# Kernel tuning notes

Measured on AMD Instinct MI355X. Metric: run time of the kernel, lower is better.

The kernel has to match this reference:

```python
import jax, jax.numpy as jnp
import numpy as np

N_NODES = 100000


def gcn_conv(x, edge_index, W, b):
    """PyG GCNConv: add self-loops, symmetric deg^-1/2 normalization, linear."""
    n = x.shape[0]
    h = x @ W  # [N, out]
    loop = jnp.arange(n, dtype=edge_index.dtype)
    src = jnp.concatenate([edge_index[0], loop])
    dst = jnp.concatenate([edge_index[1], loop])
    deg = jax.ops.segment_sum(jnp.ones_like(dst, dtype=h.dtype), dst, num_segments=n)
    dinv = jnp.where(deg > 0, jax.lax.rsqrt(deg), 0.0)
    norm = dinv[src] * dinv[dst]  # [E+N]
    msg = h[src] * norm[:, None]  # gather + scale
    out = jax.ops.segment_sum(msg, dst, num_segments=n)  # scatter-add
    return out + b


def setup_inputs() -> dict:
    key = jax.random.key(0)
    k1, k2, k3, k4 = jax.random.split(key, 4)
    d_in, d_hid, d_out = 128, 128, 128  # output_dim // 2 = 128
    E = 1600000
    x = jax.random.normal(k1, (N_NODES, d_in), dtype=jnp.float32)
    edge_index = jax.random.randint(k2, (2, E), 0, N_NODES, dtype=jnp.int64)
    s1 = 1.0 / np.sqrt(d_in)
    s2 = 1.0 / np.sqrt(d_hid)
    W1 = jax.random.normal(k3, (d_in, d_hid), dtype=jnp.float32) * s1
    b1 = jnp.zeros((d_hid,), dtype=jnp.float32)
    W2 = jax.random.normal(k4, (d_hid, d_out), dtype=jnp.float32) * s2
    b2 = jnp.zeros((d_out,), dtype=jnp.float32)
    return {"x": x, "edge_index": edge_index, "W1": W1, "b1": b1, "W2": W2, "b2": b2}


def reference(x, edge_index, W1, b1, W2, b2):
    h = jax.nn.relu(gcn_conv(x, edge_index, W1, b1))
    # dropout(p=0.5) is identity in eval mode
    return gcn_conv(h, edge_index, W2, b2)
```

## Files before the change

### kernel.cpp

```cpp
#include <hip/hip_runtime.h>

#define D 128

typedef unsigned int uint;
typedef unsigned short ushort;
typedef __attribute__((ext_vector_type(8))) short bf16x8_t;
typedef __attribute__((ext_vector_type(4))) float f32x4_t;

#define NB 128
#define BSH 7
#define BMASK 127
#define MAXBUCK 1024

__global__ __launch_bounds__(256) void kp_hist(const int* __restrict__ dst,
                                               int* __restrict__ table,
                                               int E, int nbuck, int chunk) {
    __shared__ int h[MAXBUCK];
    int t = threadIdx.x, b = blockIdx.x;
    for (int i = t; i < nbuck; i += 256) h[i] = 0;
    __syncthreads();
    int s = b * chunk, e = min(E, s + chunk);
    for (int i = s + t; i < e; i += 256)
        atomicAdd(&h[dst[i] >> BSH], 1);
    __syncthreads();
    for (int i = t; i < nbuck; i += 256)
        table[i * NB + b] = h[i];
}

__global__ void kp_scan_table(int* __restrict__ table, int* __restrict__ btot) {
    __shared__ int s[NB];
    int t = threadIdx.x, b = blockIdx.x;
    int v = table[b * NB + t];
    s[t] = v; __syncthreads();
    for (int off = 1; off < NB; off <<= 1) {
        int x = (t >= off) ? s[t - off] : 0;
        __syncthreads();
        s[t] += x;
        __syncthreads();
    }
    table[b * NB + t] = s[t] - v;
    if (t == NB - 1) btot[b] = s[t];
}

__global__ void kp_scan_btot(const int* __restrict__ btot, int* __restrict__ bucketBase,
                             int* __restrict__ row_ptr, int nbuck, int E, int n) {
    __shared__ int s[1024];
    int t = threadIdx.x;
    int v = (t < nbuck) ? btot[t] : 0;
    s[t] = v; __syncthreads();
    for (int off = 1; off < 1024; off <<= 1) {
        int x = (t >= off) ? s[t - off] : 0;
        __syncthreads();
        s[t] += x;
        __syncthreads();
    }
    if (t < nbuck) bucketBase[t] = s[t] - v;
    if (t == 0) { bucketBase[nbuck] = E; row_ptr[n] = E; }
}

__global__ __launch_bounds__(256) void kp_scatter(const int* __restrict__ src,
                                                  const int* __restrict__ dst,
                                                  const int* __restrict__ table,
                                                  const int* __restrict__ bucketBase,
                                                  uint* __restrict__ sorted,
                                                  int E, int nbuck, int chunk) {
    __shared__ int off[MAXBUCK];
    int t = threadIdx.x, b = blockIdx.x;
    for (int i = t; i < nbuck; i += 256)
        off[i] = bucketBase[i] + table[i * NB + b];
    __syncthreads();
    int s = b * chunk, e = min(E, s + chunk);
    for (int i = s + t; i < e; i += 256) {
        int d = dst[i];
        int bk = d >> BSH;
        int slot = atomicAdd(&off[bk], 1);
        sorted[slot] = ((uint)src[i] << BSH) | (uint)(d & BMASK);
    }
}

__global__ __launch_bounds__(256) void kp_build(const uint* __restrict__ sorted,
                                                const int* __restrict__ bucketBase,
                                                int* __restrict__ row_ptr,
                                                int* __restrict__ col,
                                                float* __restrict__ dinv, int n) {
    __shared__ int cnt[128], loc[128], cnt2[128];
    int t = threadIdx.x, b = blockIdx.x;
    int base = bucketBase[b], end = bucketBase[b + 1];
    if (t < 128) { cnt[t] = 0; cnt2[t] = 0; }
    __syncthreads();
    for (int i = base + t; i < end; i += 256)
        atomicAdd(&cnt[sorted[i] & BMASK], 1);
    __syncthreads();
    int v = (t < 128) ? cnt[t] : 0;
    if (t < 128) loc[t] = v;
    __syncthreads();
    for (int off = 1; off < 128; off <<= 1) {
        int x = (t >= off && t < 128) ? loc[t - off] : 0;
        __syncthreads();
        if (t < 128) loc[t] += x;
        __syncthreads();
    }
    int node = (b << BSH) + t;
    if (t < 128 && node < n) {
        row_ptr[node] = base + loc[t] - v;
        dinv[node] = rsqrtf((float)(v + 1));
    }
    __syncthreads();
    for (int i = base + t; i < end; i += 256) {
        uint p = sorted[i];
        int low = p & BMASK;
        int r = atomicAdd(&cnt2[low], 1);
        col[base + (loc[low] - cnt[low]) + r] = (int)(p >> BSH);
    }
}

__device__ inline uint bf16rn(float f) {
    uint u = __float_as_uint(f);
    return (u + 0x7fffu + ((u >> 16) & 1u)) >> 16;
}

__device__ inline void accum_bf16x8(float* a, uint4 v) {
    a[0] += __uint_as_float(v.x << 16);
    a[1] += __uint_as_float(v.x & 0xffff0000u);
    a[2] += __uint_as_float(v.y << 16);
    a[3] += __uint_as_float(v.y & 0xffff0000u);
    a[4] += __uint_as_float(v.z << 16);
    a[5] += __uint_as_float(v.z & 0xffff0000u);
    a[6] += __uint_as_float(v.w << 16);
    a[7] += __uint_as_float(v.w & 0xffff0000u);
}

__global__ void k_prep_w(const float* __restrict__ W, ushort* __restrict__ Wh,
                         ushort* __restrict__ Wl) {
    int i = blockIdx.x * blockDim.x + threadIdx.x;
    int k = i >> 7, n = i & 127;
    float w = W[k * D + n];
    uint hb = bf16rn(w);
    float hf = __uint_as_float(hb << 16);
    uint lb = bf16rn(w - hf);
    Wh[n * D + k] = (ushort)hb;
    Wl[n * D + k] = (ushort)lb;
}

template <bool A_FP32>
__global__ __launch_bounds__(256, 2) void k_gemm_mfma(const void* __restrict__ A,
                                                      const ushort* __restrict__ Wth,
                                                      const ushort* __restrict__ Wtl,
                                                      const float* __restrict__ dinv,
                                                      ushort* __restrict__ Yb, int M) {
    constexpr int STR = 72;
    constexpr int TILE = 128 * STR;
    __shared__ ushort lds[A_FP32 ? 4 * TILE : 3 * TILE];
    ushort* Ah = lds;
    ushort* Wh = lds + TILE;
    ushort* Wl = lds + 2 * TILE;
    ushort* Al = A_FP32 ? (lds + 3 * TILE) : nullptr;

    int t = threadIdx.x;
    int lane = t & 63, wave = t >> 6;
    int quad = lane >> 4, l16 = lane & 15;
    int m_off = (wave & 1) * 64;
    int n_off = (wave >> 1) * 64;
    int block_row = blockIdx.x * 128;

    f32x4_t acc[4][4];
#pragma unroll
    for (int mt = 0; mt < 4; mt++)
#pragma unroll
        for (int nt = 0; nt < 4; nt++) acc[mt][nt] = (f32x4_t){0.f, 0.f, 0.f, 0.f};

    for (int kc = 0; kc < 128; kc += 64) {
        if (A_FP32) {
            const float* Af = (const float*)A;
#pragma unroll
            for (int it = 0; it < 8; it++) {
                int s = t + it * 256;
                int row = s >> 4, kl = (s & 15) * 4;
                int gr = block_row + row;
                float4 v = make_float4(0.f, 0.f, 0.f, 0.f);
                if (gr < M) v = *(const float4*)(Af + (size_t)gr * D + kc + kl);
                ushort4 h, l;
                uint hb, lb; float hf;
                hb = bf16rn(v.x); hf = __uint_as_float(hb << 16); lb = bf16rn(v.x - hf);
                h.x = (ushort)hb; l.x = (ushort)lb;
                hb = bf16rn(v.y); hf = __uint_as_float(hb << 16); lb = bf16rn(v.y - hf);
                h.y = (ushort)hb; l.y = (ushort)lb;
                hb = bf16rn(v.z); hf = __uint_as_float(hb << 16); lb = bf16rn(v.z - hf);
                h.z = (ushort)hb; l.z = (ushort)lb;
                hb = bf16rn(v.w); hf = __uint_as_float(hb << 16); lb = bf16rn(v.w - hf);
                h.w = (ushort)hb; l.w = (ushort)lb;
                *(ushort4*)&Ah[row * STR + kl] = h;
                *(ushort4*)&Al[row * STR + kl] = l;
            }
        } else {
            const ushort* Ab = (const ushort*)A;
#pragma unroll
            for (int it = 0; it < 4; it++) {
                int s = t + it * 256;
                int row = s >> 3, kl = (s & 7) * 8;
                int gr = block_row + row;
                uint4 v = make_uint4(0u, 0u, 0u, 0u);
                if (gr < M) v = *(const uint4*)(Ab + (size_t)gr * D + kc + kl);
                *(uint4*)&Ah[row * STR + kl] = v;
            }
        }
#pragma unroll
        for (int it = 0; it < 4; it++) {
            int s = t + it * 256;
            int nrow = s >> 3, kl = (s & 7) * 8;
            *(uint4*)&Wh[nrow * STR + kl] = *(const uint4*)(Wth + nrow * D + kc + kl);
            *(uint4*)&Wl[nrow * STR + kl] = *(const uint4*)(Wtl + nrow * D + kc + kl);
        }
        __syncthreads();

#pragma unroll
        for (int ks = 0; ks < 2; ks++) {
            int kf = ks * 32 + quad * 8;
            bf16x8_t ah[4], bh[4], bl[4];
#pragma unroll
            for (int mt = 0; mt < 4; mt++)
                ah[mt] = *(const bf16x8_t*)&Ah[(m_off + mt * 16 + l16) * STR + kf];
#pragma unroll
            for (int nt = 0; nt < 4; nt++) {
                bh[nt] = *(const bf16x8_t*)&Wh[(n_off + nt * 16 + l16) * STR + kf];
                bl[nt] = *(const bf16x8_t*)&Wl[(n_off + nt * 16 + l16) * STR + kf];
            }
            if (A_FP32) {
                bf16x8_t al[4];
#pragma unroll
                for (int mt = 0; mt < 4; mt++)
                    al[mt] = *(const bf16x8_t*)&Al[(m_off + mt * 16 + l16) * STR + kf];
#pragma unroll
                for (int mt = 0; mt < 4; mt++)
#pragma unroll
                    for (int nt = 0; nt < 4; nt++) {
                        acc[mt][nt] = __builtin_amdgcn_mfma_f32_16x16x32_bf16(ah[mt], bh[nt], acc[mt][nt], 0, 0, 0);
                        acc[mt][nt] = __builtin_amdgcn_mfma_f32_16x16x32_bf16(al[mt], bh[nt], acc[mt][nt], 0, 0, 0);
                        acc[mt][nt] = __builtin_amdgcn_mfma_f32_16x16x32_bf16(ah[mt], bl[nt], acc[mt][nt], 0, 0, 0);
                    }
            } else {
#pragma unroll
                for (int mt = 0; mt < 4; mt++)
#pragma unroll
                    for (int nt = 0; nt < 4; nt++) {
                        acc[mt][nt] = __builtin_amdgcn_mfma_f32_16x16x32_bf16(ah[mt], bh[nt], acc[mt][nt], 0, 0, 0);
                        acc[mt][nt] = __builtin_amdgcn_mfma_f32_16x16x32_bf16(ah[mt], bl[nt], acc[mt][nt], 0, 0, 0);
                    }
            }
        }
        __syncthreads();
    }

#pragma unroll
    for (int mt = 0; mt < 4; mt++) {
#pragma unroll
        for (int reg = 0; reg < 4; reg++) {
            int gr = block_row + m_off + mt * 16 + quad * 4 + reg;
            if (gr < M) {
                float di = dinv[gr];
#pragma unroll
                for (int nt = 0; nt < 4; nt++) {
                    int colg = n_off + nt * 16 + l16;
                    Yb[(size_t)gr * D + colg] = (ushort)bf16rn(di * acc[mt][nt][reg]);
                }
            }
        }
    }
}

__global__ __launch_bounds__(256) void k_agg(const ushort* __restrict__ Hb,
                                             const int* __restrict__ row_ptr,
                                             const int* __restrict__ col,
                                             const float* __restrict__ dinv,
                                             const float* __restrict__ bias,
                                             float* __restrict__ Yf, ushort* __restrict__ Yb,
                                             int n, int do_relu, int out_bf16) {
    int node = blockIdx.x * 4 + (threadIdx.x >> 6);
    int lane = threadIdx.x & 63;
    int chain = lane >> 4;
    int l16   = lane & 15;
    if (node >= n) return;

    int start = row_ptr[node];
    int end   = row_ptr[node + 1];

    float a0[8], a1[8];
#pragma unroll
    for (int k = 0; k < 8; k++) { a0[k] = 0.f; a1[k] = 0.f; }

    if (chain == 0) {
        uint4 v = ((const uint4*)(Hb + (size_t)node * D))[l16];
        accum_bf16x8(a0, v);
    }

    int e = start + chain;
    for (; e + 4 < end; e += 8) {
        int s0 = col[e];
        int s1 = col[e + 4];
        uint4 v0 = ((const uint4*)(Hb + (size_t)s0 * D))[l16];
        uint4 v1 = ((const uint4*)(Hb + (size_t)s1 * D))[l16];
        accum_bf16x8(a0, v0);
        accum_bf16x8(a1, v1);
    }
    if (e < end) {
        int s0 = col[e];
        uint4 v0 = ((const uint4*)(Hb + (size_t)s0 * D))[l16];
        accum_bf16x8(a0, v0);
    }

    float acc[8];
#pragma unroll
    for (int k = 0; k < 8; k++) {
        float v = a0[k] + a1[k];
        v += __shfl_xor(v, 16, 64);
        v += __shfl_xor(v, 32, 64);
        acc[k] = v;
    }

    if (chain == 0) {
        float di = dinv[node];
        const float4* bp = (const float4*)bias + l16 * 2;
        float4 b0 = bp[0], b1 = bp[1];
        float o[8];
        o[0] = fmaf(di, acc[0], b0.x); o[1] = fmaf(di, acc[1], b0.y);
        o[2] = fmaf(di, acc[2], b0.z); o[3] = fmaf(di, acc[3], b0.w);
        o[4] = fmaf(di, acc[4], b1.x); o[5] = fmaf(di, acc[5], b1.y);
        o[6] = fmaf(di, acc[6], b1.z); o[7] = fmaf(di, acc[7], b1.w);
        if (do_relu) {
#pragma unroll
            for (int k = 0; k < 8; k++) o[k] = fmaxf(o[k], 0.f);
        }
        if (out_bf16) {
            uint4 pk;
            pk.x = bf16rn(o[0]) | (bf16rn(o[1]) << 16);
            pk.y = bf16rn(o[2]) | (bf16rn(o[3]) << 16);
            pk.z = bf16rn(o[4]) | (bf16rn(o[5]) << 16);
            pk.w = bf16rn(o[6]) | (bf16rn(o[7]) << 16);
            ((uint4*)(Yb + (size_t)node * D))[l16] = pk;
        } else {
            float4* yp = (float4*)(Yf + (size_t)node * D) + l16 * 2;
            yp[0] = make_float4(o[0], o[1], o[2], o[3]);
            yp[1] = make_float4(o[4], o[5], o[6], o[7]);
        }
    }
}

extern "C" void kernel_launch(void* const* d_in, const int* in_sizes, int n_in,
                              void* d_out, int out_size, void* d_ws, size_t ws_size,
                              hipStream_t stream) {
    const float* x  = (const float*)d_in[0];
    const int*   ei = (const int*)d_in[1];
    const float* W1 = (const float*)d_in[2];
    const float* b1 = (const float*)d_in[3];
    const float* W2 = (const float*)d_in[4];
    const float* b2 = (const float*)d_in[5];
    float* out = (float*)d_out;

    int n = in_sizes[0] / D;
    int E = in_sizes[1] / 2;
    const int* src = ei;
    const int* dst = ei + E;

    char* p = (char*)d_ws;
    ushort* h_buf = (ushort*)p; p += (size_t)n * D * sizeof(ushort);
    ushort* y_buf = (ushort*)p; p += (size_t)n * D * sizeof(ushort);
    ushort* w1h   = (ushort*)p; p += (size_t)D * D * sizeof(ushort);
    ushort* w1l   = (ushort*)p; p += (size_t)D * D * sizeof(ushort);
    ushort* w2h   = (ushort*)p; p += (size_t)D * D * sizeof(ushort);
    ushort* w2l   = (ushort*)p; p += (size_t)D * D * sizeof(ushort);
    float* dinv   = (float*)p;  p += (size_t)n * sizeof(float);
    int*   row_ptr= (int*)p;    p += (size_t)(n + 1) * sizeof(int);
    int*   table  = (int*)p;    p += (size_t)MAXBUCK * NB * sizeof(int);
    int*   btot   = (int*)p;    p += (size_t)MAXBUCK * sizeof(int);
    int*   bbase  = (int*)p;    p += (size_t)(MAXBUCK + 1) * sizeof(int);
    uint*  sorted = (uint*)p;   p += (size_t)E * sizeof(uint);
    int*   col    = (int*)p;    p += (size_t)E * sizeof(int);

    int nbuck = (n + BMASK) >> BSH;
    int chunk = (E + NB - 1) / NB;

    kp_hist<<<NB, 256, 0, stream>>>(dst, table, E, nbuck, chunk);
    kp_scan_table<<<nbuck, NB, 0, stream>>>(table, btot);
    kp_scan_btot<<<1, 1024, 0, stream>>>(btot, bbase, row_ptr, nbuck, E, n);
    kp_scatter<<<NB, 256, 0, stream>>>(src, dst, table, bbase, sorted, E, nbuck, chunk);
    kp_build<<<nbuck, 256, 0, stream>>>(sorted, bbase, row_ptr, col, dinv, n);

    k_prep_w<<<(D * D) / 256, 256, 0, stream>>>(W1, w1h, w1l);
    k_prep_w<<<(D * D) / 256, 256, 0, stream>>>(W2, w2h, w2l);

    int gemm_grid = (n + 127) / 128;
    int agg_grid  = (n + 3) / 4;

    k_gemm_mfma<true><<<gemm_grid, 256, 0, stream>>>(x, w1h, w1l, dinv, h_buf, n);
    k_agg<<<agg_grid, 256, 0, stream>>>(h_buf, row_ptr, col, dinv, b1, nullptr, y_buf, n, 1, 1);
    k_gemm_mfma<false><<<gemm_grid, 256, 0, stream>>>(y_buf, w2h, w2l, dinv, h_buf, n);
    k_agg<<<agg_grid, 256, 0, stream>>>(h_buf, row_ptr, col, dinv, b2, out, nullptr, n, 0, 0);
}
```

Measured before the change: 353.3 us.

## Replace sort-based CSR build with fixed-capacity bucket scatter and unroll aggregation

Replaces the histogram/scan/scatter/build pipeline with a single global-atomic scatter into fixed-capacity per-bucket arrays, then sorts each bucket in LDS and writes column indices in place, using separate row start/end arrays. Merges the two weight-prep kernels, widens the aggregation loop to four independent gather chains, and uses nontemporal stores for the final fp32 output. This removes several kernel launches and scan passes. The capacity limit risks silently dropping edges if a bucket overflows, and global atomics may contend.

```diff
diff --git a/kernel.cpp b/kernel.cpp
--- a/kernel.cpp
+++ b/kernel.cpp
@@ -7,89 +7,44 @@
 typedef __attribute__((ext_vector_type(8))) short bf16x8_t;
 typedef __attribute__((ext_vector_type(4))) float f32x4_t;
 
-#define NB 128
 #define BSH 7
 #define BMASK 127
-#define MAXBUCK 1024
-
-__global__ __launch_bounds__(256) void kp_hist(const int* __restrict__ dst,
-                                               int* __restrict__ table,
-                                               int E, int nbuck, int chunk) {
-    __shared__ int h[MAXBUCK];
-    int t = threadIdx.x, b = blockIdx.x;
-    for (int i = t; i < nbuck; i += 256) h[i] = 0;
-    __syncthreads();
-    int s = b * chunk, e = min(E, s + chunk);
-    for (int i = s + t; i < e; i += 256)
-        atomicAdd(&h[dst[i] >> BSH], 1);
-    __syncthreads();
-    for (int i = t; i < nbuck; i += 256)
-        table[i * NB + b] = h[i];
-}
-
-__global__ void kp_scan_table(int* __restrict__ table, int* __restrict__ btot) {
-    __shared__ int s[NB];
-    int t = threadIdx.x, b = blockIdx.x;
-    int v = table[b * NB + t];
-    s[t] = v; __syncthreads();
-    for (int off = 1; off < NB; off <<= 1) {
-        int x = (t >= off) ? s[t - off] : 0;
-        __syncthreads();
-        s[t] += x;
-        __syncthreads();
-    }
-    table[b * NB + t] = s[t] - v;
-    if (t == NB - 1) btot[b] = s[t];
-}
-
-__global__ void kp_scan_btot(const int* __restrict__ btot, int* __restrict__ bucketBase,
-                             int* __restrict__ row_ptr, int nbuck, int E, int n) {
-    __shared__ int s[1024];
-    int t = threadIdx.x;
-    int v = (t < nbuck) ? btot[t] : 0;
-    s[t] = v; __syncthreads();
-    for (int off = 1; off < 1024; off <<= 1) {
-        int x = (t >= off) ? s[t - off] : 0;
-        __syncthreads();
-        s[t] += x;
-        __syncthreads();
-    }
-    if (t < nbuck) bucketBase[t] = s[t] - v;
-    if (t == 0) { bucketBase[nbuck] = E; row_ptr[n] = E; }
-}
-
-__global__ __launch_bounds__(256) void kp_scatter(const int* __restrict__ src,
-                                                  const int* __restrict__ dst,
-                                                  const int* __restrict__ table,
-                                                  const int* __restrict__ bucketBase,
-                                                  uint* __restrict__ sorted,
-                                                  int E, int nbuck, int chunk) {
-    __shared__ int off[MAXBUCK];
-    int t = threadIdx.x, b = blockIdx.x;
-    for (int i = t; i < nbuck; i += 256)
-        off[i] = bucketBase[i] + table[i * NB + b];
-    __syncthreads();
-    int s = b * chunk, e = min(E, s + chunk);
-    for (int i = s + t; i < e; i += 256) {
-        int d = dst[i];
-        int bk = d >> BSH;
-        int slot = atomicAdd(&off[bk], 1);
-        sorted[slot] = ((uint)src[i] << BSH) | (uint)(d & BMASK);
-    }
-}
-
-__global__ __launch_bounds__(256) void kp_build(const uint* __restrict__ sorted,
-                                                const int* __restrict__ bucketBase,
-                                                int* __restrict__ row_ptr,
-                                                int* __restrict__ col,
-                                                float* __restrict__ dinv, int n) {
+#define CAP 4096
+#define GSTRIDE 16
+
+__global__ __launch_bounds__(256) void kp_scatter2(const int* __restrict__ src,
+                                                   const int* __restrict__ dst,
+                                                   int* __restrict__ gcnt,
+                                                   uint* __restrict__ bkt, int E) {
+    int i = (blockIdx.x * 256 + threadIdx.x) * 2;
+    if (i >= E) return;
+    int d0 = dst[i], s0 = src[i];
+    int bk0 = d0 >> BSH;
+    int slot0 = atomicAdd(&gcnt[bk0 * GSTRIDE], 1);
+    if (slot0 < CAP) bkt[(size_t)bk0 * CAP + slot0] = ((uint)s0 << BSH) | (uint)(d0 & BMASK);
+    if (i + 1 < E) {
+        int d1 = dst[i + 1], s1 = src[i + 1];
+        int bk1 = d1 >> BSH;
+        int slot1 = atomicAdd(&gcnt[bk1 * GSTRIDE], 1);
+        if (slot1 < CAP) bkt[(size_t)bk1 * CAP + slot1] = ((uint)s1 << BSH) | (uint)(d1 & BMASK);
+    }
+}
+
+__global__ __launch_bounds__(256) void kp_build2(uint* __restrict__ bkt,
+                                                 const int* __restrict__ gcnt,
+                                                 int* __restrict__ row_start,
+                                                 int* __restrict__ row_end,
+                                                 float* __restrict__ dinv, int n) {
+    __shared__ uint ents[CAP];
     __shared__ int cnt[128], loc[128], cnt2[128];
     int t = threadIdx.x, b = blockIdx.x;
-    int base = bucketBase[b], end = bucketBase[b + 1];
+    int m = gcnt[b * GSTRIDE];
+    if (m > CAP) m = CAP;
+    uint* bk = bkt + (size_t)b * CAP;
+    for (int i = t; i < m; i += 256) ents[i] = bk[i];
     if (t < 128) { cnt[t] = 0; cnt2[t] = 0; }
     __syncthreads();
-    for (int i = base + t; i < end; i += 256)
-        atomicAdd(&cnt[sorted[i] & BMASK], 1);
+    for (int i = t; i < m; i += 256) atomicAdd(&cnt[ents[i] & BMASK], 1);
     __syncthreads();
     int v = (t < 128) ? cnt[t] : 0;
     if (t < 128) loc[t] = v;
@@ -100,17 +55,19 @@
         if (t < 128) loc[t] += x;
         __syncthreads();
     }
+    int base = b * CAP;
     int node = (b << BSH) + t;
     if (t < 128 && node < n) {
-        row_ptr[node] = base + loc[t] - v;
+        row_start[node] = base + loc[t] - v;
+        row_end[node]   = base + loc[t];
         dinv[node] = rsqrtf((float)(v + 1));
     }
     __syncthreads();
-    for (int i = base + t; i < end; i += 256) {
-        uint p = sorted[i];
+    for (int i = t; i < m; i += 256) {
+        uint p = ents[i];
         int low = p & BMASK;
         int r = atomicAdd(&cnt2[low], 1);
-        col[base + (loc[low] - cnt[low]) + r] = (int)(p >> BSH);
+        ((int*)bk)[(loc[low] - cnt[low]) + r] = (int)(p >> BSH);
     }
 }
 
@@ -130,16 +87,20 @@
     a[7] += __uint_as_float(v.w & 0xffff0000u);
 }
 
-__global__ void k_prep_w(const float* __restrict__ W, ushort* __restrict__ Wh,
-                         ushort* __restrict__ Wl) {
+__global__ void k_prep_w2(const float* __restrict__ W1, const float* __restrict__ W2,
+                          ushort* __restrict__ W1h, ushort* __restrict__ W1l,
+                          ushort* __restrict__ W2h, ushort* __restrict__ W2l) {
     int i = blockIdx.x * blockDim.x + threadIdx.x;
-    int k = i >> 7, n = i & 127;
-    float w = W[k * D + n];
+    int sel = i >> 14;
+    int j = i & 16383;
+    int k = j >> 7, nn = j & 127;
+    const float* W = sel ? W2 : W1;
+    float w = W[k * D + nn];
     uint hb = bf16rn(w);
     float hf = __uint_as_float(hb << 16);
     uint lb = bf16rn(w - hf);
-    Wh[n * D + k] = (ushort)hb;
-    Wl[n * D + k] = (ushort)lb;
+    if (sel) { W2h[nn * D + k] = (ushort)hb; W2l[nn * D + k] = (ushort)lb; }
+    else     { W1h[nn * D + k] = (ushort)hb; W1l[nn * D + k] = (ushort)lb; }
 }
 
 template <bool A_FP32>
@@ -269,7 +230,8 @@
 }
 
 __global__ __launch_bounds__(256) void k_agg(const ushort* __restrict__ Hb,
-                                             const int* __restrict__ row_ptr,
+                                             const int* __restrict__ row_start,
+                                             const int* __restrict__ row_end,
                                              const int* __restrict__ col,
                                              const float* __restrict__ dinv,
                                              const float* __restrict__ bias,
@@ -281,37 +243,45 @@
     int l16   = lane & 15;
     if (node >= n) return;
 
-    int start = row_ptr[node];
-    int end   = row_ptr[node + 1];
-
-    float a0[8], a1[8];
-#pragma unroll
-    for (int k = 0; k < 8; k++) { a0[k] = 0.f; a1[k] = 0.f; }
+    int start = row_start[node];
+    int end   = row_end[node];
+
+    float a0[8], a1[8], a2[8], a3[8];
+#pragma unroll
+    for (int k = 0; k < 8; k++) { a0[k] = 0.f; a1[k] = 0.f; a2[k] = 0.f; a3[k] = 0.f; }
+
+    const uint4* hb = (const uint4*)Hb;
 
     if (chain == 0) {
-        uint4 v = ((const uint4*)(Hb + (size_t)node * D))[l16];
+        uint4 v = hb[(size_t)node * 16 + l16];
         accum_bf16x8(a0, v);
     }
 
     int e = start + chain;
-    for (; e + 4 < end; e += 8) {
+    for (; e + 12 < end; e += 16) {
         int s0 = col[e];
         int s1 = col[e + 4];
-        uint4 v0 = ((const uint4*)(Hb + (size_t)s0 * D))[l16];
-        uint4 v1 = ((const uint4*)(Hb + (size_t)s1 * D))[l16];
+        int s2 = col[e + 8];
+        int s3 = col[e + 12];
+        uint4 v0 = hb[(size_t)s0 * 16 + l16];
+        uint4 v1 = hb[(size_t)s1 * 16 + l16];
+        uint4 v2 = hb[(size_t)s2 * 16 + l16];
+        uint4 v3 = hb[(size_t)s3 * 16 + l16];
         accum_bf16x8(a0, v0);
         accum_bf16x8(a1, v1);
-    }
-    if (e < end) {
+        accum_bf16x8(a2, v2);
+        accum_bf16x8(a3, v3);
+    }
+    for (; e < end; e += 4) {
         int s0 = col[e];
-        uint4 v0 = ((const uint4*)(Hb + (size_t)s0 * D))[l16];
+        uint4 v0 = hb[(size_t)s0 * 16 + l16];
         accum_bf16x8(a0, v0);
     }
 
     float acc[8];
 #pragma unroll
     for (int k = 0; k < 8; k++) {
-        float v = a0[k] + a1[k];
+        float v = (a0[k] + a1[k]) + (a2[k] + a3[k]);
         v += __shfl_xor(v, 16, 64);
         v += __shfl_xor(v, 32, 64);
         acc[k] = v;
@@ -338,9 +308,11 @@
             pk.w = bf16rn(o[6]) | (bf16rn(o[7]) << 16);
             ((uint4*)(Yb + (size_t)node * D))[l16] = pk;
         } else {
-            float4* yp = (float4*)(Yf + (size_t)node * D) + l16 * 2;
-            yp[0] = make_float4(o[0], o[1], o[2], o[3]);
-            yp[1] = make_float4(o[4], o[5], o[6], o[7]);
+            f32x4_t q0 = {o[0], o[1], o[2], o[3]};
+            f32x4_t q1 = {o[4], o[5], o[6], o[7]};
+            f32x4_t* yp = (f32x4_t*)(Yf + (size_t)node * D) + l16 * 2;
+            __builtin_nontemporal_store(q0, yp);
+            __builtin_nontemporal_store(q1, yp + 1);
         }
     }
 }
@@ -361,6 +333,8 @@
     const int* src = ei;
     const int* dst = ei + E;
 
+    int nbuck = (n + BMASK) >> BSH;
+
     char* p = (char*)d_ws;
     ushort* h_buf = (ushort*)p; p += (size_t)n * D * sizeof(ushort);
     ushort* y_buf = (ushort*)p; p += (size_t)n * D * sizeof(ushort);
@@ -368,31 +342,24 @@
     ushort* w1l   = (ushort*)p; p += (size_t)D * D * sizeof(ushort);
     ushort* w2h   = (ushort*)p; p += (size_t)D * D * sizeof(ushort);
     ushort* w2l   = (ushort*)p; p += (size_t)D * D * sizeof(ushort);
+    uint*  bkt    = (uint*)p;   p += (size_t)nbuck * CAP * sizeof(uint);
     float* dinv   = (float*)p;  p += (size_t)n * sizeof(float);
-    int*   row_ptr= (int*)p;    p += (size_t)(n + 1) * sizeof(int);
-    int*   table  = (int*)p;    p += (size_t)MAXBUCK * NB * sizeof(int);
-    int*   btot   = (int*)p;    p += (size_t)MAXBUCK * sizeof(int);
-    int*   bbase  = (int*)p;    p += (size_t)(MAXBUCK + 1) * sizeof(int);
-    uint*  sorted = (uint*)p;   p += (size_t)E * sizeof(uint);
-    int*   col    = (int*)p;    p += (size_t)E * sizeof(int);
-
-    int nbuck = (n + BMASK) >> BSH;
-    int chunk = (E + NB - 1) / NB;
-
-    kp_hist<<<NB, 256, 0, stream>>>(dst, table, E, nbuck, chunk);
-    kp_scan_table<<<nbuck, NB, 0, stream>>>(table, btot);
-    kp_scan_btot<<<1, 1024, 0, stream>>>(btot, bbase, row_ptr, nbuck, E, n);
-    kp_scatter<<<NB, 256, 0, stream>>>(src, dst, table, bbase, sorted, E, nbuck, chunk);
-    kp_build<<<nbuck, 256, 0, stream>>>(sorted, bbase, row_ptr, col, dinv, n);
-
-    k_prep_w<<<(D * D) / 256, 256, 0, stream>>>(W1, w1h, w1l);
-    k_prep_w<<<(D * D) / 256, 256, 0, stream>>>(W2, w2h, w2l);
+    int*   row_s  = (int*)p;    p += (size_t)n * sizeof(int);
+    int*   row_e  = (int*)p;    p += (size_t)n * sizeof(int);
+    int*   gcnt   = (int*)p;    p += (size_t)nbuck * GSTRIDE * sizeof(int);
+
+    (void)hipMemsetAsync(gcnt, 0, (size_t)nbuck * GSTRIDE * sizeof(int), stream);
+    kp_scatter2<<<(E + 511) / 512, 256, 0, stream>>>(src, dst, gcnt, bkt, E);
+    kp_build2<<<nbuck, 256, 0, stream>>>(bkt, gcnt, row_s, row_e, dinv, n);
+
+    k_prep_w2<<<128, 256, 0, stream>>>(W1, W2, w1h, w1l, w2h, w2l);
 
     int gemm_grid = (n + 127) / 128;
     int agg_grid  = (n + 3) / 4;
+    const int* colp = (const int*)bkt;
 
     k_gemm_mfma<true><<<gemm_grid, 256, 0, stream>>>(x, w1h, w1l, dinv, h_buf, n);
-    k_agg<<<agg_grid, 256, 0, stream>>>(h_buf, row_ptr, col, dinv, b1, nullptr, y_buf, n, 1, 1);
+    k_agg<<<agg_grid, 256, 0, stream>>>(h_buf, row_s, row_e, colp, dinv, b1, nullptr, y_buf, n, 1, 1);
     k_gemm_mfma<false><<<gemm_grid, 256, 0, stream>>>(y_buf, w2h, w2l, dinv, h_buf, n);
-    k_agg<<<agg_grid, 256, 0, stream>>>(h_buf, row_ptr, col, dinv, b2, out, nullptr, n, 0, 0);
-}
+    k_agg<<<agg_grid, 256, 0, stream>>>(h_buf, row_s, row_e, colp, dinv, b2, out, nullptr, n, 0, 0);
+}
```

Result: slower. 397.9 us (+12.6%).
